# Kernel tuning notes

Measured on AMD Instinct MI355X. Metric: run time of the kernel, lower is better.

Reference implementation:

```python
import jax, jax.numpy as jnp
import numpy as np

D_HALF = 255
H = 2 * D_HALF + 1   # 511 channels (2*d+1)
L = 2048             # sequence length
N = 32               # S4D complex state modes per channel
NLAYERS = 4          # l
EPS = 1e-5


def setup_inputs() -> dict:
    key = jax.random.key(0)
    ks = jax.random.split(key, 10)
    Z = jax.random.normal(ks[0], (H, L), dtype=jnp.float32)
    # S4D-Lin initialization
    dt_min, dt_max = 1e-3, 1e-1
    log_dt = (jax.random.uniform(ks[1], (H,), dtype=jnp.float32)
              * (np.log(dt_max) - np.log(dt_min)) + np.log(dt_min))
    A_real_log = jnp.log(0.5 * jnp.ones((H, N), dtype=jnp.float32))
    A_imag = jnp.pi * jnp.broadcast_to(jnp.arange(N, dtype=jnp.float32), (H, N))
    C_re = jax.random.normal(ks[2], (H, N), dtype=jnp.float32)
    C_im = jax.random.normal(ks[3], (H, N), dtype=jnp.float32)
    D_skip = jax.random.normal(ks[4], (H,), dtype=jnp.float32)
    glu_w = jax.random.normal(ks[5], (2 * H, H), dtype=jnp.float32) / np.sqrt(H)
    glu_b = jnp.zeros((2 * H,), dtype=jnp.float32)
    ln_g = jnp.ones((H,), dtype=jnp.float32)
    ln_b = jnp.zeros((H,), dtype=jnp.float32)
    return {"Z": Z, "log_dt": log_dt, "A_real_log": A_real_log, "A_imag": A_imag,
            "C_re": C_re, "C_im": C_im, "D_skip": D_skip,
            "glu_w": glu_w, "glu_b": glu_b, "ln_g": ln_g, "ln_b": ln_b}


def _s4d_kernel(log_dt, A_real_log, A_imag, C_re, C_im):
    # A: (H,N) complex with negative real part; ZOH discretization kernel
    A = -jnp.exp(A_real_log) + 1j * A_imag
    dtA = A * jnp.exp(log_dt)[:, None]                  # (H,N)
    Ccoef = (C_re + 1j * C_im) * (jnp.exp(dtA) - 1.0) / A  # (H,N)
    V = jnp.exp(dtA[:, :, None] * jnp.arange(L, dtype=jnp.float32))  # (H,N,L)
    return 2.0 * jnp.einsum('hn,hnl->hl', Ccoef, V).real  # (H,L)


def _s4_block(Z, K, D_skip, glu_w, glu_b):
    # Z: (B,H,L); causal FFT convolution with kernel K (H,L)
    n = 2 * L
    Kf = jnp.fft.rfft(K, n=n)                  # (H, L+1)
    Uf = jnp.fft.rfft(Z, n=n)                  # (B,H,L+1)
    y = jnp.fft.irfft(Uf * Kf, n=n)[..., :L]   # (B,H,L)
    y = y + D_skip[:, None] * Z
    y = jax.nn.gelu(y)
    # output 1x1 conv H -> 2H followed by GLU over channels
    y2 = jnp.einsum('oh,bhl->bol', glu_w, y) + glu_b[:, None]
    return y2[:, :H] * jax.nn.sigmoid(y2[:, H:])


def _layernorm_channels(Z, g, b):
    # LayerNorm over the channel dim (module does norm(Z.transpose(-1,-2)).transpose(-1,-2))
    zt = jnp.swapaxes(Z, -1, -2)               # (B,L,H)
    mu = jnp.mean(zt, axis=-1, keepdims=True)
    var = jnp.mean((zt - mu) ** 2, axis=-1, keepdims=True)
    zt = (zt - mu) * jax.lax.rsqrt(var + EPS) * g + b
    return jnp.swapaxes(zt, -1, -2)


def reference(Z, log_dt, A_real_log, A_imag, C_re, C_im, D_skip, glu_w, glu_b, ln_g, ln_b):
    K = _s4d_kernel(log_dt, A_real_log, A_imag, C_re, C_im)
    z = Z[None]                                # unsqueeze(0) -> (1,H,L)
    for _ in range(NLAYERS):                   # mode='auto': shared layer, l iterations
        residual = z
        z = _s4_block(z, K, D_skip, glu_w, glu_b)
        z = z + residual
        z = _layernorm_channels(z, ln_g, ln_b)
    return z[0]                                # squeeze(0) -> (H,L)
```

## Files before the change

### kernel.cpp

```cpp
#include <hip/hip_runtime.h>
#include <hip/hip_bf16.h>
#include <math.h>

#define H 511
#define L 2048
#define NST 32
#define NLAYERS 4
#define LN_EPS 1e-5f
#define NCH 32
#define TC (L / NCH)
#define HN (H * NST)
#define HP 512
#define GBK 64
#define GBN 64
#define NSTRIPE 16

typedef __attribute__((ext_vector_type(8))) short short8;
typedef __attribute__((ext_vector_type(4))) float f32x4;

__device__ __forceinline__ ushort f2bf(float v) {
    __hip_bfloat16 b = __float2bfloat16(v);
    return *reinterpret_cast<ushort*>(&b);
}

__global__ __launch_bounds__(256) void pre_kernel(
    const float* __restrict__ log_dt,
    const float* __restrict__ A_real_log,
    const float* __restrict__ A_imag,
    const float* __restrict__ C_re,
    const float* __restrict__ C_im,
    const float* __restrict__ W,
    float* __restrict__ wr_o, float* __restrict__ wi_o,
    float* __restrict__ cr_o, float* __restrict__ ci_o,
    ushort* __restrict__ wbf)
{
    int idx = blockIdx.x * blockDim.x + threadIdx.x;
    if (idx < HN) {
        int h = idx / NST;
        float Ar = -expf(A_real_log[idx]);
        float Ai = A_imag[idx];
        float dt = expf(log_dt[h]);
        float dr = Ar * dt, di = Ai * dt;
        float er = expf(dr);
        float wr = er * cosf(di);
        float wi = er * sinf(di);
        float den = Ar * Ar + Ai * Ai;
        float a = wr - 1.0f, b = wi;
        float inv = 1.0f / den;
        float qr = (a * Ar + b * Ai) * inv;
        float qi = (b * Ar - a * Ai) * inv;
        wr_o[idx] = wr; wi_o[idx] = wi;
        cr_o[idx] = 2.0f * (C_re[idx] * qr - C_im[idx] * qi);
        ci_o[idx] = 2.0f * (C_re[idx] * qi + C_im[idx] * qr);
    }
    if (idx < 2 * H * HP) {
        int r = idx / HP, k = idx % HP;
        float v = (k < H) ? W[(size_t)r * H + k] : 0.0f;
        wbf[idx] = f2bf(v);
    }
}

template <int CTRL, int ROW_MASK>
__device__ __forceinline__ float dpp_add(float x) {
    int r = __builtin_amdgcn_update_dpp(0, __float_as_int(x), CTRL, ROW_MASK, 0xf, true);
    return x + __int_as_float(r);
}
__device__ __forceinline__ float reduce32_to_lane31(float p) {
    p = dpp_add<0x111, 0xf>(p);
    p = dpp_add<0x112, 0xf>(p);
    p = dpp_add<0x114, 0xf>(p);
    p = dpp_add<0x118, 0xf>(p);
    p = dpp_add<0x142, 0xa>(p);
    return p;
}

__device__ __forceinline__ float gelu_tanh(float v) {
    const float c0 = 0.7978845608028654f;
    float t = tanhf(c0 * (v + 0.044715f * v * v * v));
    return 0.5f * v * (1.0f + t);
}

__global__ __launch_bounds__(1024) void conv_fused(
    const float* __restrict__ z,
    const float* __restrict__ wr_,
    const float* __restrict__ wi_,
    const float* __restrict__ cr_,
    const float* __restrict__ ci_,
    const float* __restrict__ D_skip,
    ushort* __restrict__ yb)
{
    __shared__ float zs[L];
    __shared__ float ber[NCH][NST];
    __shared__ float bei[NCH][NST];
    __shared__ float ysf[L];

    const int tid  = threadIdx.x;
    const int wv   = tid >> 6;
    const int half = (tid >> 5) & 1;
    const int ln   = tid & 31;
    const int c    = wv * 2 + half;
    const int h    = blockIdx.x;

    *(float2*)&zs[tid * 2] = *(const float2*)&z[(size_t)h * L + tid * 2];

    const int cidx = h * NST + ln;
    const float wr = wr_[cidx], wi = wi_[cidx];
    const float cr = cr_[cidx], ci = ci_[cidx];
    const float Dh = D_skip[h];
    __syncthreads();

    float sr = 0.f, si = 0.f;
    {
        const float* zp = &zs[c * TC];
        #pragma unroll 4
        for (int l = 0; l < TC; ++l) {
            float zl = zp[l];
            float nsr = fmaf(wr, sr, fmaf(-wi, si, zl));
            float nsi = fmaf(wr, si, wi * sr);
            sr = nsr; si = nsi;
        }
    }
    ber[c][ln] = sr;
    bei[c][ln] = si;
    __syncthreads();

    if (tid < 32) {
        float wtr = wr, wti = wi;
        #pragma unroll
        for (int k = 0; k < 6; ++k) {
            float nr = wtr * wtr - wti * wti;
            float ni = 2.0f * wtr * wti;
            wtr = nr; wti = ni;
        }
        float er = 0.f, ei = 0.f;
        #pragma unroll
        for (int cc = 0; cc < NCH; ++cc) {
            float s_r = ber[cc][tid], s_i = bei[cc][tid];
            ber[cc][tid] = er; bei[cc][tid] = ei;
            float ner = fmaf(wtr, er, fmaf(-wti, ei, s_r));
            float nei = fmaf(wtr, ei, fmaf(wti, er, s_i));
            er = ner; ei = nei;
        }
    }
    __syncthreads();

    sr = ber[c][ln];
    si = bei[c][ln];
    {
        const float* zp = &zs[c * TC];
        float* yp = &ysf[c * TC];
        for (int l = 0; l < TC; ++l) {
            float zl = zp[l];
            float nsr = fmaf(wr, sr, fmaf(-wi, si, zl));
            float nsi = fmaf(wr, si, wi * sr);
            sr = nsr; si = nsi;
            float p = fmaf(cr, sr, -ci * si);
            p = reduce32_to_lane31(p);
            if (ln == 31) yp[l] = fmaf(Dh, zl, p);
        }
    }
    __syncthreads();

    {
        ushort2 v;
        v.x = f2bf(gelu_tanh(ysf[tid * 2]));
        v.y = f2bf(gelu_tanh(ysf[tid * 2 + 1]));
        *(ushort2*)&yb[(size_t)h * L + tid * 2] = v;
    }
}

__global__ __launch_bounds__(256) void ytr_kernel(
    const ushort* __restrict__ yb,
    ushort* __restrict__ ytb)
{
    __shared__ ushort t[32][34];
    const int tx = threadIdx.x;
    const int ty = threadIdx.y;
    const int l0 = blockIdx.x * 32;
    const int h0 = blockIdx.y * 32;
    #pragma unroll
    for (int j = 0; j < 4; ++j) {
        int h = h0 + ty + j * 8;
        ushort v = 0;
        if (h < H) v = yb[(size_t)h * L + l0 + tx];
        t[tx][ty + j * 8] = v;
    }
    __syncthreads();
    #pragma unroll
    for (int j = 0; j < 4; ++j) {
        int l = l0 + ty + j * 8;
        ytb[(size_t)l * HP + h0 + tx] = t[ty + j * 8][tx];
    }
}

__global__ __launch_bounds__(256) void glu_mfma(
    const ushort* __restrict__ wbf,
    const ushort* __restrict__ ytb,
    const float* __restrict__ bias,
    const float* __restrict__ zres,
    float* __restrict__ out)
{
    __shared__ ushort As1[32 * GBK];
    __shared__ ushort As2[32 * GBK];
    __shared__ ushort Bs[GBN * GBK];

    const int tid = threadIdx.x;
    const int h0 = blockIdx.y * 32;
    const int l0 = blockIdx.x * GBN;
    const int wid = tid >> 6;
    const int lane = tid & 63;
    const int wrow = (wid >> 1) * 16;
    const int wcol = (wid & 1) * 32;

    f32x4 acc1[2] = {{0.f,0.f,0.f,0.f},{0.f,0.f,0.f,0.f}};
    f32x4 acc2[2] = {{0.f,0.f,0.f,0.f},{0.f,0.f,0.f,0.f}};

    const int ar = tid >> 3;
    const int ak = tid & 7;
    const int hq1 = (h0 + ar < H) ? (h0 + ar) : (H - 1);
    const int hq2 = hq1 + H;
    const int aswz = ak ^ (ar & 7);

    for (int k0 = 0; k0 < HP; k0 += GBK) {
        short8 va1 = *(const short8*)&wbf[(size_t)hq1 * HP + k0 + ak * 8];
        short8 va2 = *(const short8*)&wbf[(size_t)hq2 * HP + k0 + ak * 8];
        *(short8*)&As1[ar * GBK + aswz * 8] = va1;
        *(short8*)&As2[ar * GBK + aswz * 8] = va2;
        #pragma unroll
        for (int j = 0; j < 2; ++j) {
            int idx = tid + j * 256;
            int br = idx >> 3;
            int bk = idx & 7;
            short8 vb = *(const short8*)&ytb[(size_t)(l0 + br) * HP + k0 + bk * 8];
            *(short8*)&Bs[br * GBK + (bk ^ (br & 7)) * 8] = vb;
        }
        __syncthreads();

        #pragma unroll
        for (int kk = 0; kk < 2; ++kk) {
            const int arow = wrow + (lane & 15);
            const int kg = kk * 4 + (lane >> 4);
            short8 a1 = *(const short8*)&As1[arow * GBK + (kg ^ (arow & 7)) * 8];
            short8 a2 = *(const short8*)&As2[arow * GBK + (kg ^ (arow & 7)) * 8];
            #pragma unroll
            for (int nf = 0; nf < 2; ++nf) {
                const int brow = wcol + nf * 16 + (lane & 15);
                short8 b = *(const short8*)&Bs[brow * GBK + (kg ^ (brow & 7)) * 8];
                acc1[nf] = __builtin_amdgcn_mfma_f32_16x16x32_bf16(a1, b, acc1[nf], 0, 0, 0);
                acc2[nf] = __builtin_amdgcn_mfma_f32_16x16x32_bf16(a2, b, acc2[nf], 0, 0, 0);
            }
        }
        __syncthreads();
    }

    #pragma unroll
    for (int nf = 0; nf < 2; ++nf) {
        const int col = l0 + wcol + nf * 16 + (lane & 15);
        #pragma unroll
        for (int r = 0; r < 4; ++r) {
            const int h = h0 + wrow + (lane >> 4) * 4 + r;
            if (h < H) {
                float v1 = acc1[nf][r] + bias[h];
                float v2 = acc2[nf][r] + bias[h + H];
                float g = v1 * (1.0f / (1.0f + expf(-v2)));
                out[(size_t)h * L + col] = g + zres[(size_t)h * L + col];
            }
        }
    }
}

__global__ __launch_bounds__(256) void ln_stats(
    const float* __restrict__ zpre,
    float* __restrict__ psum, float* __restrict__ psq)
{
    __shared__ float ss[4][64];
    __shared__ float sg[4][64];
    const int tx = threadIdx.x & 63;
    const int ty = threadIdx.x >> 6;
    const int l = blockIdx.x * 64 + tx;
    const int s = blockIdx.y;
    const int hbase = s * 32;

    float sum = 0.f, sq = 0.f;
    #pragma unroll
    for (int j = 0; j < 8; ++j) {
        int h = hbase + ty + j * 4;
        if (h < H) {
            float v = zpre[(size_t)h * L + l];
            sum += v;
            sq = fmaf(v, v, sq);
        }
    }
    ss[ty][tx] = sum;
    sg[ty][tx] = sq;
    __syncthreads();
    if (ty == 0) {
        psum[(size_t)s * L + l] = ss[0][tx] + ss[1][tx] + ss[2][tx] + ss[3][tx];
        psq[(size_t)s * L + l]  = sg[0][tx] + sg[1][tx] + sg[2][tx] + sg[3][tx];
    }
}

__global__ __launch_bounds__(256) void ln_apply(
    const float* __restrict__ zpre,
    const float* __restrict__ psum, const float* __restrict__ psq,
    const float* __restrict__ g, const float* __restrict__ b,
    float* __restrict__ out)
{
    const int tx = threadIdx.x & 63;
    const int ty = threadIdx.x >> 6;
    const int l = blockIdx.x * 64 + tx;
    const int s = blockIdx.y;

    float S = 0.f, Q = 0.f;
    #pragma unroll
    for (int k = 0; k < NSTRIPE; ++k) {
        S += psum[(size_t)k * L + l];
        Q += psq[(size_t)k * L + l];
    }
    const float invH = 1.0f / (float)H;
    float mu = S * invH;
    float var = Q * invH - mu * mu;
    float rstd = rsqrtf(var + LN_EPS);

    const int hbase = s * 32;
    #pragma unroll
    for (int j = 0; j < 8; ++j) {
        int h = hbase + ty + j * 4;
        if (h < H) {
            float v = zpre[(size_t)h * L + l];
            out[(size_t)h * L + l] = (v - mu) * rstd * g[h] + b[h];
        }
    }
}

extern "C" void kernel_launch(void* const* d_in, const int* in_sizes, int n_in,
                              void* d_out, int out_size, void* d_ws, size_t ws_size,
                              hipStream_t stream) {
    const float* Z          = (const float*)d_in[0];
    const float* log_dt     = (const float*)d_in[1];
    const float* A_real_log = (const float*)d_in[2];
    const float* A_imag     = (const float*)d_in[3];
    const float* C_re       = (const float*)d_in[4];
    const float* C_im       = (const float*)d_in[5];
    const float* D_skip     = (const float*)d_in[6];
    const float* glu_w      = (const float*)d_in[7];
    const float* glu_b      = (const float*)d_in[8];
    const float* ln_g       = (const float*)d_in[9];
    const float* ln_b       = (const float*)d_in[10];

    float* out = (float*)d_out;
    float* ws  = (float*)d_ws;

    float* wr   = ws;
    float* wi   = wr + HN;
    float* cr   = wi + HN;
    float* ci   = cr + HN;
    float* zbuf = ci + HN;
    float* psum = zbuf + (size_t)H * L;
    float* psq  = psum + (size_t)NSTRIPE * L;
    ushort* yb  = (ushort*)(psq + (size_t)NSTRIPE * L);
    ushort* ytb = yb + (size_t)H * L;
    ushort* wbf = ytb + (size_t)L * HP;

    pre_kernel<<<(2 * H * HP + 255) / 256, 256, 0, stream>>>(
        log_dt, A_real_log, A_imag, C_re, C_im, glu_w,
        wr, wi, cr, ci, wbf);

    const dim3 tg(L / 32, HP / 32);
    const dim3 tb(32, 8);
    const dim3 gg(L / GBN, (H + 31) / 32);
    const dim3 lg(L / 64, NSTRIPE);

    for (int layer = 0; layer < NLAYERS; ++layer) {
        const float* zcur = (layer == 0) ? Z : zbuf;

        conv_fused<<<H, 1024, 0, stream>>>(
            zcur, wr, wi, cr, ci, D_skip, yb);
        ytr_kernel<<<tg, tb, 0, stream>>>(yb, ytb);
        glu_mfma<<<gg, 256, 0, stream>>>(wbf, ytb, glu_b, zcur, out);

        float* lnout = (layer < NLAYERS - 1) ? zbuf : out;
        ln_stats<<<lg, 256, 0, stream>>>(out, psum, psq);
        ln_apply<<<lg, 256, 0, stream>>>(out, psum, psq, ln_g, ln_b, lnout);
    }
}
```

Baseline: 240.3 us.

## Fuse transpose and LayerNorm statistics into GLU MFMA kernel

```diff
diff --git a/kernel.cpp b/kernel.cpp
--- a/kernel.cpp
+++ b/kernel.cpp
@@ -169,40 +169,21 @@
     }
 }
 
-__global__ __launch_bounds__(256) void ytr_kernel(
-    const ushort* __restrict__ yb,
-    ushort* __restrict__ ytb)
-{
-    __shared__ ushort t[32][34];
-    const int tx = threadIdx.x;
-    const int ty = threadIdx.y;
-    const int l0 = blockIdx.x * 32;
-    const int h0 = blockIdx.y * 32;
-    #pragma unroll
-    for (int j = 0; j < 4; ++j) {
-        int h = h0 + ty + j * 8;
-        ushort v = 0;
-        if (h < H) v = yb[(size_t)h * L + l0 + tx];
-        t[tx][ty + j * 8] = v;
-    }
-    __syncthreads();
-    #pragma unroll
-    for (int j = 0; j < 4; ++j) {
-        int l = l0 + ty + j * 8;
-        ytb[(size_t)l * HP + h0 + tx] = t[ty + j * 8][tx];
-    }
-}
-
 __global__ __launch_bounds__(256) void glu_mfma(
     const ushort* __restrict__ wbf,
-    const ushort* __restrict__ ytb,
+    const ushort* __restrict__ yb,
     const float* __restrict__ bias,
     const float* __restrict__ zres,
-    float* __restrict__ out)
+    float* __restrict__ out,
+    float* __restrict__ psum,
+    float* __restrict__ psq)
 {
     __shared__ ushort As1[32 * GBK];
     __shared__ ushort As2[32 * GBK];
     __shared__ ushort Bs[GBN * GBK];
+    __shared__ ushort tempT[4][32 * 40];
+    __shared__ float  sls[2][64];
+    __shared__ float  slq[2][64];
 
     const int tid = threadIdx.x;
     const int h0 = blockIdx.y * 32;
@@ -221,18 +202,47 @@
     const int hq2 = hq1 + H;
     const int aswz = ak ^ (ar & 7);
 
+    const int tm   = tid >> 6;
+    const int t64  = tid & 63;
+    const int ksub = (tm & 1) * 32;
+    const int lsub = (tm >> 1) * 32;
+    const int bkl  = t64 >> 1;
+    const int bhalf= t64 & 1;
+    const int blr  = t64 >> 1;
+    const int bkh  = t64 & 1;
+
     for (int k0 = 0; k0 < HP; k0 += GBK) {
-        short8 va1 = *(const short8*)&wbf[(size_t)hq1 * HP + k0 + ak * 8];
-        short8 va2 = *(const short8*)&wbf[(size_t)hq2 * HP + k0 + ak * 8];
-        *(short8*)&As1[ar * GBK + aswz * 8] = va1;
-        *(short8*)&As2[ar * GBK + aswz * 8] = va2;
-        #pragma unroll
-        for (int j = 0; j < 2; ++j) {
-            int idx = tid + j * 256;
-            int br = idx >> 3;
-            int bk = idx & 7;
-            short8 vb = *(const short8*)&ytb[(size_t)(l0 + br) * HP + k0 + bk * 8];
-            *(short8*)&Bs[br * GBK + (bk ^ (br & 7)) * 8] = vb;
+        {
+            short8 va1 = *(const short8*)&wbf[(size_t)hq1 * HP + k0 + ak * 8];
+            short8 va2 = *(const short8*)&wbf[(size_t)hq2 * HP + k0 + ak * 8];
+            *(short8*)&As1[ar * GBK + aswz * 8] = va1;
+            *(short8*)&As2[ar * GBK + aswz * 8] = va2;
+        }
+        {
+            const int kg = k0 + ksub + bkl;
+            short8 v0 = {0,0,0,0,0,0,0,0}, v1 = {0,0,0,0,0,0,0,0};
+            if (kg < H) {
+                const ushort* row = &yb[(size_t)kg * L + l0 + lsub + bhalf * 16];
+                v0 = *(const short8*)&row[0];
+                v1 = *(const short8*)&row[8];
+            }
+            ushort* tp = &tempT[tm][0];
+            #pragma unroll
+            for (int j = 0; j < 8; ++j)
+                tp[(bhalf * 16 + j) * 40 + bkl] = (ushort)v0[j];
+            #pragma unroll
+            for (int j = 0; j < 8; ++j)
+                tp[(bhalf * 16 + 8 + j) * 40 + bkl] = (ushort)v1[j];
+        }
+        __syncthreads();
+        {
+            const ushort* tp = &tempT[tm][0];
+            short8 b0 = *(const short8*)&tp[blr * 40 + bkh * 16];
+            short8 b1 = *(const short8*)&tp[blr * 40 + bkh * 16 + 8];
+            const int L_ = lsub + blr;
+            const int kg0 = (ksub >> 3) + bkh * 2;
+            *(short8*)&Bs[L_ * GBK + ((kg0    ) ^ (L_ & 7)) * 8] = b0;
+            *(short8*)&Bs[L_ * GBK + ((kg0 + 1) ^ (L_ & 7)) * 8] = b1;
         }
         __syncthreads();
 
@@ -253,6 +263,7 @@
         __syncthreads();
     }
 
+    float ps[2] = {0.f, 0.f}, pq[2] = {0.f, 0.f};
     #pragma unroll
     for (int nf = 0; nf < 2; ++nf) {
         const int col = l0 + wcol + nf * 16 + (lane & 15);
@@ -262,41 +273,29 @@
             if (h < H) {
                 float v1 = acc1[nf][r] + bias[h];
                 float v2 = acc2[nf][r] + bias[h + H];
-                float g = v1 * (1.0f / (1.0f + expf(-v2)));
-                out[(size_t)h * L + col] = g + zres[(size_t)h * L + col];
+                float o = v1 * (1.0f / (1.0f + expf(-v2))) + zres[(size_t)h * L + col];
+                out[(size_t)h * L + col] = o;
+                ps[nf] += o;
+                pq[nf] = fmaf(o, o, pq[nf]);
             }
         }
     }
-}
-
-__global__ __launch_bounds__(256) void ln_stats(
-    const float* __restrict__ zpre,
-    float* __restrict__ psum, float* __restrict__ psq)
-{
-    __shared__ float ss[4][64];
-    __shared__ float sg[4][64];
-    const int tx = threadIdx.x & 63;
-    const int ty = threadIdx.x >> 6;
-    const int l = blockIdx.x * 64 + tx;
-    const int s = blockIdx.y;
-    const int hbase = s * 32;
-
-    float sum = 0.f, sq = 0.f;
     #pragma unroll
-    for (int j = 0; j < 8; ++j) {
-        int h = hbase + ty + j * 4;
-        if (h < H) {
-            float v = zpre[(size_t)h * L + l];
-            sum += v;
-            sq = fmaf(v, v, sq);
-        }
-    }
-    ss[ty][tx] = sum;
-    sg[ty][tx] = sq;
-    __syncthreads();
-    if (ty == 0) {
-        psum[(size_t)s * L + l] = ss[0][tx] + ss[1][tx] + ss[2][tx] + ss[3][tx];
-        psq[(size_t)s * L + l]  = sg[0][tx] + sg[1][tx] + sg[2][tx] + sg[3][tx];
+    for (int nf = 0; nf < 2; ++nf) {
+        ps[nf] += __shfl_xor(ps[nf], 16, 64);
+        ps[nf] += __shfl_xor(ps[nf], 32, 64);
+        pq[nf] += __shfl_xor(pq[nf], 16, 64);
+        pq[nf] += __shfl_xor(pq[nf], 32, 64);
+        if ((lane >> 4) == 0) {
+            int cl = wcol + nf * 16 + lane;
+            sls[wid >> 1][cl] = ps[nf];
+            slq[wid >> 1][cl] = pq[nf];
+        }
+    }
+    __syncthreads();
+    if (tid < 64) {
+        psum[(size_t)blockIdx.y * L + l0 + tid] = sls[0][tid] + sls[1][tid];
+        psq [(size_t)blockIdx.y * L + l0 + tid] = slq[0][tid] + slq[1][tid];
     }
 }
 
@@ -359,15 +358,12 @@
     float* psum = zbuf + (size_t)H * L;
     float* psq  = psum + (size_t)NSTRIPE * L;
     ushort* yb  = (ushort*)(psq + (size_t)NSTRIPE * L);
-    ushort* ytb = yb + (size_t)H * L;
-    ushort* wbf = ytb + (size_t)L * HP;
+    ushort* wbf = yb + (size_t)H * L;
 
     pre_kernel<<<(2 * H * HP + 255) / 256, 256, 0, stream>>>(
         log_dt, A_real_log, A_imag, C_re, C_im, glu_w,
         wr, wi, cr, ci, wbf);
 
-    const dim3 tg(L / 32, HP / 32);
-    const dim3 tb(32, 8);
     const dim3 gg(L / GBN, (H + 31) / 32);
     const dim3 lg(L / 64, NSTRIPE);
 
@@ -376,11 +372,9 @@
 
         conv_fused<<<H, 1024, 0, stream>>>(
             zcur, wr, wi, cr, ci, D_skip, yb);
-        ytr_kernel<<<tg, tb, 0, stream>>>(yb, ytb);
-        glu_mfma<<<gg, 256, 0, stream>>>(wbf, ytb, glu_b, zcur, out);
+        glu_mfma<<<gg, 256, 0, stream>>>(wbf, yb, glu_b, zcur, out, psum, psq);
 
         float* lnout = (layer < NLAYERS - 1) ? zbuf : out;
-        ln_stats<<<lg, 256, 0, stream>>>(out, psum, psq);
         ln_apply<<<lg, 256, 0, stream>>>(out, psum, psq, ln_g, ln_b, lnout);
     }
 }
```

Result: faster. 222.6 us (-7.4%).
